# Optimization experiments

Measured on AMD Instinct MI355X. Metric: run time of the kernel, lower is better.

The kernel has to match this reference:

```python
import jax, jax.numpy as jnp
import numpy as np

N_NODES = 100000

def setup_inputs() -> dict:
    key = jax.random.key(0)
    k1, k2 = jax.random.split(key)
    node_features = jax.random.normal(k1, (N_NODES, 64), dtype=jnp.float32)
    edge_index = jax.random.randint(k2, (2, 1600000), 0, N_NODES, dtype=jnp.int64)
    return {"node_features": node_features, "edge_index": edge_index}


def reference(node_features, edge_index):
    # Gather: [E, d] source and destination node features
    src = node_features[edge_index[0]]
    dest = node_features[edge_index[1]]
    # Message: m_ij = src + dest   (minimal concrete message fn)
    messages = src + dest
    num_nodes = node_features.shape[0]
    target = edge_index[1]
    # Aggregate: scatter-add over destination node (index_add equivalent)
    aggregated = jax.ops.segment_sum(messages, target, num_segments=num_nodes)
    # aggr == 'mean': divide by in-degree, clamped at 1
    ones = jnp.ones((messages.shape[0],), dtype=messages.dtype)
    counts = jax.ops.segment_sum(ones, target, num_segments=num_nodes)
    aggregated = aggregated / jnp.clip(counts, 1.0)[:, None]
    # Update: residual (shapes match, no batchnorm/dropout)
    return node_features + aggregated
```

## Files before the change

### kernel.cpp

```cpp
#include <hip/hip_runtime.h>


#define D 64
#define NPB 32
#define NPB_SHIFT 5
#define SRC_BITS 17
#define CAP 768
#define K_BLOCKS 256
#define K_THREADS 512
#define CHUNK 1024


__global__ void detect_idx_width(const int* __restrict__ ei, int* __restrict__ flag) {
    unsigned long long nz = __ballot(ei[2 * (int)threadIdx.x + 1] != 0);
    if (threadIdx.x == 0) *flag = (nz == 0ULL) ? 1 : 0;
}

__device__ __forceinline__ int load_src(const int* ei, int e, int n_edges, bool is64) {
    return is64 ? ei[2 * (size_t)e] : ei[e];
}
__device__ __forceinline__ int load_tgt(const int* ei, int e, int n_edges, bool is64) {
    return is64 ? ei[2 * ((size_t)n_edges + e)] : ei[(size_t)n_edges + e];
}


__global__ __launch_bounds__(K_THREADS) void place_padded(
        const int* __restrict__ ei, const int* __restrict__ flag,
        int* __restrict__ gcnt, int* __restrict__ bucket, int n_edges, int nb) {
    extern __shared__ int sh[];
    int* lhist = sh;
    int* lbase = sh + nb;
    int* lcur  = sh + 2 * nb;
    const bool is64 = (*flag != 0);
    const int epb = (n_edges + gridDim.x - 1) / gridDim.x;
    const int e0 = blockIdx.x * epb;
    const int e1 = min(n_edges, e0 + epb);

    for (int i = threadIdx.x; i < nb; i += blockDim.x) { lhist[i] = 0; lcur[i] = 0; }
    __syncthreads();
    for (int e = e0 + threadIdx.x; e < e1; e += blockDim.x)
        atomicAdd(&lhist[load_tgt(ei, e, n_edges, is64) >> NPB_SHIFT], 1);
    __syncthreads();
    for (int b = threadIdx.x; b < nb; b += blockDim.x) {
        int c = lhist[b];
        lbase[b] = c ? (b * CAP + atomicAdd(&gcnt[b], c)) : 0;
    }
    __syncthreads();
    for (int e = e0 + threadIdx.x; e < e1; e += blockDim.x) {
        int s = load_src(ei, e, n_edges, is64);
        int t = load_tgt(ei, e, n_edges, is64);
        int b = t >> NPB_SHIFT;
        int pos = lbase[b] + atomicAdd(&lcur[b], 1);
        if (pos < (b + 1) * CAP)
            bucket[pos] = ((t & (NPB - 1)) << SRC_BITS) | s;
    }
}


__global__ __launch_bounds__(256) void bucket_aggregate(
        const float* __restrict__ nf, const int* __restrict__ gcnt,
        const int* __restrict__ bucket, float* __restrict__ out, int n_nodes) {
    __shared__ int st[CHUNK];
    __shared__ int srt[CHUNK];
    __shared__ int bins[NPB], ofs[NPB], cur[NPB];
    const int blk = blockIdx.x;
    const int base = blk * NPB;
    const int tid = threadIdx.x;
    const int wid = tid >> 6;
    const int lane = tid & 63;
    const int SMASK = (1 << SRC_BITS) - 1;

    float acc[8];
    int cnt[8];
#pragma unroll
    for (int k = 0; k < 8; ++k) { acc[k] = 0.f; cnt[k] = 0; }

    const int s0 = blk * CAP;
    const int m = min(gcnt[blk], CAP);

    for (int done = 0; done < m; done += CHUNK) {
        const int mc = min(CHUNK, m - done);
        if (tid < NPB) bins[tid] = 0;
        __syncthreads();
        for (int i = tid; i < mc; i += 256) {
            int p = bucket[s0 + done + i];
            st[i] = p;
            atomicAdd(&bins[p >> SRC_BITS], 1);
        }
        __syncthreads();
        if (tid < NPB) {
            int v = bins[tid];
            int incl = v;
#pragma unroll
            for (int off = 1; off < NPB; off <<= 1) {
                int up = __shfl_up(incl, off, NPB);
                if (tid >= off) incl += up;
            }
            ofs[tid] = incl - v;
            cur[tid] = incl - v;
        }
        __syncthreads();
        for (int i = tid; i < mc; i += 256) {
            int p = st[i];
            int b = p >> SRC_BITS;
            int pos = atomicAdd(&cur[b], 1);
            srt[pos] = p & SMASK;
        }
        __syncthreads();
#pragma unroll
        for (int k = 0; k < 8; ++k) {
            int r = (wid << 3) + k;
            int j0 = ofs[r];
            int n = bins[r];
            int j1 = j0 + n;
            cnt[k] += n;
            int j = j0;
            for (; j + 8 <= j1; j += 8) {
                int a0 = srt[j],     a1 = srt[j + 1], a2 = srt[j + 2], a3 = srt[j + 3];
                int a4 = srt[j + 4], a5 = srt[j + 5], a6 = srt[j + 6], a7 = srt[j + 7];
                float v0 = nf[(size_t)a0 * D + lane];
                float v1 = nf[(size_t)a1 * D + lane];
                float v2 = nf[(size_t)a2 * D + lane];
                float v3 = nf[(size_t)a3 * D + lane];
                float v4 = nf[(size_t)a4 * D + lane];
                float v5 = nf[(size_t)a5 * D + lane];
                float v6 = nf[(size_t)a6 * D + lane];
                float v7 = nf[(size_t)a7 * D + lane];
                acc[k] += v0; acc[k] += v1; acc[k] += v2; acc[k] += v3;
                acc[k] += v4; acc[k] += v5; acc[k] += v6; acc[k] += v7;
            }
            for (; j + 4 <= j1; j += 4) {
                int a0 = srt[j], a1 = srt[j + 1], a2 = srt[j + 2], a3 = srt[j + 3];
                float v0 = nf[(size_t)a0 * D + lane];
                float v1 = nf[(size_t)a1 * D + lane];
                float v2 = nf[(size_t)a2 * D + lane];
                float v3 = nf[(size_t)a3 * D + lane];
                acc[k] += v0; acc[k] += v1; acc[k] += v2; acc[k] += v3;
            }
            for (; j < j1; ++j) acc[k] += nf[(size_t)srt[j] * D + lane];
        }
        __syncthreads();
    }

#pragma unroll
    for (int k = 0; k < 8; ++k) {
        int node = base + (wid << 3) + k;
        if (node < n_nodes) {
            float c = (float)cnt[k];
            float self = nf[(size_t)node * D + lane];
            float scale = (c > 0.f) ? 2.0f : 1.0f;
            float inv = (c > 0.f) ? (1.0f / c) : 1.0f;
            out[(size_t)node * D + lane] = self * scale + acc[k] * inv;
        }
    }
}


__global__ __launch_bounds__(256) void edge_scatter(
        const float* __restrict__ nf, const int* __restrict__ ei,
        const int* __restrict__ flag, float* __restrict__ agg,
        int* __restrict__ cnt, int n_edges) {
    const bool is64 = (*flag != 0);
    const int lane = threadIdx.x & 63;
    const int wave = (int)((blockIdx.x * (unsigned)blockDim.x + threadIdx.x) >> 6);
    const int nwaves = (int)((gridDim.x * (unsigned)blockDim.x) >> 6);
    for (int e = wave; e < n_edges; e += nwaves) {
        int s = load_src(ei, e, n_edges, is64);
        int t = load_tgt(ei, e, n_edges, is64);
        atomicAdd(&agg[(size_t)t * D + lane], nf[(size_t)s * D + lane]);
        if (lane == 0) atomicAdd(&cnt[t], 1);
    }
}

__global__ __launch_bounds__(256) void finalize(
        const float* __restrict__ nf, const int* __restrict__ cnt,
        float* __restrict__ out, int n_elems) {
    int i = blockIdx.x * blockDim.x + threadIdx.x;
    if (i >= n_elems) return;
    int v = i >> 6;
    float c = (float)cnt[v];
    float inv = (c > 0.f) ? (1.0f / c) : 1.0f;
    float scale = (c > 0.f) ? 2.0f : 1.0f;
    out[i] = nf[i] * scale + out[i] * inv;
}


extern "C" void kernel_launch(void* const* d_in, const int* in_sizes, int n_in,
                              void* d_out, int out_size, void* d_ws, size_t ws_size,
                              hipStream_t stream) {
    const float* nf = (const float*)d_in[0];
    const int* ei = (const int*)d_in[1];
    float* out = (float*)d_out;

    const int n_nodes = in_sizes[0] / D;
    const int n_edges = in_sizes[1] / 2;

    const int nb = (n_nodes + NPB - 1) / NPB;

    int* gcnt   = (int*)d_ws;
    int* flag   = gcnt + nb;
    int* bucket = flag + 1;
    const size_t need = ((size_t)nb * CAP + nb + 1) * sizeof(int);
    const size_t place_lds = (size_t)3 * nb * sizeof(int);

    if (ws_size >= need && n_nodes <= (1 << SRC_BITS) && place_lds <= 64 * 1024) {
        hipMemsetAsync(gcnt, 0, (size_t)nb * sizeof(int), stream);
        detect_idx_width<<<1, 64, 0, stream>>>(ei, flag);
        place_padded<<<K_BLOCKS, K_THREADS, place_lds, stream>>>(
            ei, flag, gcnt, bucket, n_edges, nb);
        bucket_aggregate<<<nb, 256, 0, stream>>>(nf, gcnt, bucket, out, n_nodes);
    } else {
        hipMemsetAsync(d_out, 0, (size_t)out_size * sizeof(float), stream);
        hipMemsetAsync(d_ws, 0, ((size_t)n_nodes + 1) * sizeof(int), stream);
        int* fcnt = (int*)d_ws;
        int* fflag = fcnt + n_nodes;
        detect_idx_width<<<1, 64, 0, stream>>>(ei, fflag);
        edge_scatter<<<2048, 256, 0, stream>>>(nf, ei, fflag, out, fcnt, n_edges);
        finalize<<<(n_nodes * D + 255) / 256, 256, 0, stream>>>(nf, fcnt, out, n_nodes * D);
    }
}
```

Baseline: 170.0 us.

## Use two-level coarse bucketing with per-block fine filtering and XCD-aware block mapping

Edges are placed into 196 coarse buckets of 512 target nodes instead of ~3125 fine buckets of 32, so the placement kernel keeps tiny static LDS histograms and issues fewer global atomics. The index-width detection moves into the placement kernel, removing one launch. Each aggregate block then scans the whole coarse bucket (about 8K entries) and ballot-compacts only the entries for its 32 nodes, which multiplies bucket reads by 16 in exchange for cheaper placement. Block IDs are remapped so consecutive fine blocks land on the same XCD, aiming for L2 reuse of the shared coarse bucket.

```diff
diff --git a/kernel.cpp b/kernel.cpp
--- a/kernel.cpp
+++ b/kernel.cpp
@@ -2,13 +2,15 @@
 
 
 #define D 64
-#define NPB 32
-#define NPB_SHIFT 5
+#define CSHIFT 9
+#define CNODES 512
+#define FSHIFT 5
+#define FNODES 32
 #define SRC_BITS 17
-#define CAP 768
+#define CAPC 9216
+#define CAPF 768
 #define K_BLOCKS 256
 #define K_THREADS 512
-#define CHUNK 1024
 
 
 __global__ void detect_idx_width(const int* __restrict__ ei, int* __restrict__ flag) {
@@ -24,132 +26,154 @@
 }
 
 
-__global__ __launch_bounds__(K_THREADS) void place_padded(
-        const int* __restrict__ ei, const int* __restrict__ flag,
-        int* __restrict__ gcnt, int* __restrict__ bucket, int n_edges, int nb) {
-    extern __shared__ int sh[];
-    int* lhist = sh;
-    int* lbase = sh + nb;
-    int* lcur  = sh + 2 * nb;
-    const bool is64 = (*flag != 0);
+__global__ __launch_bounds__(K_THREADS) void place_coarse(
+        const int* __restrict__ ei, int* __restrict__ gcnt,
+        int* __restrict__ bucket, int n_edges, int ncoarse) {
+    __shared__ int lhist[256], lbase[256], lcur[256];
+    __shared__ int is64_sh;
+    const int tid = threadIdx.x;
+    if (tid < 64) {
+        unsigned long long nz = __ballot(ei[2 * tid + 1] != 0);
+        if (tid == 0) is64_sh = (nz == 0ULL) ? 1 : 0;
+    }
+    for (int i = tid; i < ncoarse; i += blockDim.x) { lhist[i] = 0; lcur[i] = 0; }
+    __syncthreads();
+    const bool is64 = (is64_sh != 0);
     const int epb = (n_edges + gridDim.x - 1) / gridDim.x;
     const int e0 = blockIdx.x * epb;
     const int e1 = min(n_edges, e0 + epb);
 
-    for (int i = threadIdx.x; i < nb; i += blockDim.x) { lhist[i] = 0; lcur[i] = 0; }
-    __syncthreads();
-    for (int e = e0 + threadIdx.x; e < e1; e += blockDim.x)
-        atomicAdd(&lhist[load_tgt(ei, e, n_edges, is64) >> NPB_SHIFT], 1);
-    __syncthreads();
-    for (int b = threadIdx.x; b < nb; b += blockDim.x) {
+    for (int e = e0 + tid; e < e1; e += blockDim.x)
+        atomicAdd(&lhist[load_tgt(ei, e, n_edges, is64) >> CSHIFT], 1);
+    __syncthreads();
+    for (int b = tid; b < ncoarse; b += blockDim.x) {
         int c = lhist[b];
-        lbase[b] = c ? (b * CAP + atomicAdd(&gcnt[b], c)) : 0;
-    }
-    __syncthreads();
-    for (int e = e0 + threadIdx.x; e < e1; e += blockDim.x) {
+        lbase[b] = c ? (b * CAPC + atomicAdd(&gcnt[b], c)) : 0;
+    }
+    __syncthreads();
+    for (int e = e0 + tid; e < e1; e += blockDim.x) {
         int s = load_src(ei, e, n_edges, is64);
         int t = load_tgt(ei, e, n_edges, is64);
-        int b = t >> NPB_SHIFT;
+        int b = t >> CSHIFT;
         int pos = lbase[b] + atomicAdd(&lcur[b], 1);
-        if (pos < (b + 1) * CAP)
-            bucket[pos] = ((t & (NPB - 1)) << SRC_BITS) | s;
+        if (pos < (b + 1) * CAPC)
+            bucket[pos] = ((t & (CNODES - 1)) << SRC_BITS) | s;
     }
 }
 
 
 __global__ __launch_bounds__(256) void bucket_aggregate(
         const float* __restrict__ nf, const int* __restrict__ gcnt,
-        const int* __restrict__ bucket, float* __restrict__ out, int n_nodes) {
-    __shared__ int st[CHUNK];
-    __shared__ int srt[CHUNK];
-    __shared__ int bins[NPB], ofs[NPB], cur[NPB];
-    const int blk = blockIdx.x;
-    const int base = blk * NPB;
+        const int* __restrict__ bucket, float* __restrict__ out,
+        int n_nodes, int nfine) {
+    __shared__ int stq[CAPF];
+    __shared__ int srt[CAPF];
+    __shared__ int bins[FNODES], ofs[FNODES], cur[FNODES];
+    __shared__ int mcnt_sh;
     const int tid = threadIdx.x;
     const int wid = tid >> 6;
     const int lane = tid & 63;
     const int SMASK = (1 << SRC_BITS) - 1;
 
+    const int bid = blockIdx.x;
+    const int q = nfine >> 3, r8 = nfine & 7;
+    const int xcd = bid & 7, rank = bid >> 3;
+    const int w = (xcd < r8 ? xcd * (q + 1) : r8 * (q + 1) + (xcd - r8) * q) + rank;
+
+    const int c = w >> 4;
+    const int sub = w & 15;
+    const int base = w * FNODES;
+
     float acc[8];
     int cnt[8];
 #pragma unroll
     for (int k = 0; k < 8; ++k) { acc[k] = 0.f; cnt[k] = 0; }
 
-    const int s0 = blk * CAP;
-    const int m = min(gcnt[blk], CAP);
-
-    for (int done = 0; done < m; done += CHUNK) {
-        const int mc = min(CHUNK, m - done);
-        if (tid < NPB) bins[tid] = 0;
-        __syncthreads();
-        for (int i = tid; i < mc; i += 256) {
-            int p = bucket[s0 + done + i];
-            st[i] = p;
-            atomicAdd(&bins[p >> SRC_BITS], 1);
-        }
-        __syncthreads();
-        if (tid < NPB) {
-            int v = bins[tid];
-            int incl = v;
-#pragma unroll
-            for (int off = 1; off < NPB; off <<= 1) {
-                int up = __shfl_up(incl, off, NPB);
-                if (tid >= off) incl += up;
-            }
-            ofs[tid] = incl - v;
-            cur[tid] = incl - v;
-        }
-        __syncthreads();
-        for (int i = tid; i < mc; i += 256) {
-            int p = st[i];
-            int b = p >> SRC_BITS;
-            int pos = atomicAdd(&cur[b], 1);
-            srt[pos] = p & SMASK;
-        }
-        __syncthreads();
-#pragma unroll
-        for (int k = 0; k < 8; ++k) {
-            int r = (wid << 3) + k;
-            int j0 = ofs[r];
-            int n = bins[r];
-            int j1 = j0 + n;
-            cnt[k] += n;
-            int j = j0;
-            for (; j + 8 <= j1; j += 8) {
-                int a0 = srt[j],     a1 = srt[j + 1], a2 = srt[j + 2], a3 = srt[j + 3];
-                int a4 = srt[j + 4], a5 = srt[j + 5], a6 = srt[j + 6], a7 = srt[j + 7];
-                float v0 = nf[(size_t)a0 * D + lane];
-                float v1 = nf[(size_t)a1 * D + lane];
-                float v2 = nf[(size_t)a2 * D + lane];
-                float v3 = nf[(size_t)a3 * D + lane];
-                float v4 = nf[(size_t)a4 * D + lane];
-                float v5 = nf[(size_t)a5 * D + lane];
-                float v6 = nf[(size_t)a6 * D + lane];
-                float v7 = nf[(size_t)a7 * D + lane];
-                acc[k] += v0; acc[k] += v1; acc[k] += v2; acc[k] += v3;
-                acc[k] += v4; acc[k] += v5; acc[k] += v6; acc[k] += v7;
-            }
-            for (; j + 4 <= j1; j += 4) {
-                int a0 = srt[j], a1 = srt[j + 1], a2 = srt[j + 2], a3 = srt[j + 3];
-                float v0 = nf[(size_t)a0 * D + lane];
-                float v1 = nf[(size_t)a1 * D + lane];
-                float v2 = nf[(size_t)a2 * D + lane];
-                float v3 = nf[(size_t)a3 * D + lane];
-                acc[k] += v0; acc[k] += v1; acc[k] += v2; acc[k] += v3;
-            }
-            for (; j < j1; ++j) acc[k] += nf[(size_t)srt[j] * D + lane];
-        }
-        __syncthreads();
+    if (tid == 0) mcnt_sh = 0;
+    if (tid < FNODES) bins[tid] = 0;
+    __syncthreads();
+
+    const int m = min(gcnt[c], CAPC);
+    const size_t c0 = (size_t)c * CAPC;
+    for (int i = tid; i < m; i += 256) {
+        int p = bucket[c0 + i];
+        int tl = p >> SRC_BITS;
+        bool match = ((tl >> FSHIFT) == sub);
+        unsigned long long mk = __ballot(match);
+        int wbase = 0;
+        if (lane == 0) wbase = atomicAdd(&mcnt_sh, (int)__popcll(mk));
+        wbase = __shfl(wbase, 0, 64);
+        if (match) {
+            int pos = wbase + (int)__popcll(mk & ((1ULL << lane) - 1ULL));
+            if (pos < CAPF)
+                stq[pos] = ((tl & (FNODES - 1)) << SRC_BITS) | (p & SMASK);
+        }
+    }
+    __syncthreads();
+    const int mm = min(mcnt_sh, CAPF);
+
+    for (int i = tid; i < mm; i += 256) atomicAdd(&bins[stq[i] >> SRC_BITS], 1);
+    __syncthreads();
+    if (tid < FNODES) {
+        int v = bins[tid];
+        int incl = v;
+#pragma unroll
+        for (int off = 1; off < FNODES; off <<= 1) {
+            int up = __shfl_up(incl, off, FNODES);
+            if (tid >= off) incl += up;
+        }
+        ofs[tid] = incl - v;
+        cur[tid] = incl - v;
+    }
+    __syncthreads();
+    for (int i = tid; i < mm; i += 256) {
+        int p = stq[i];
+        int pos = atomicAdd(&cur[p >> SRC_BITS], 1);
+        srt[pos] = p & SMASK;
+    }
+    __syncthreads();
+
+#pragma unroll
+    for (int k = 0; k < 8; ++k) {
+        int r = (wid << 3) + k;
+        int j0 = ofs[r];
+        int n = bins[r];
+        int j1 = j0 + n;
+        cnt[k] += n;
+        int j = j0;
+        for (; j + 8 <= j1; j += 8) {
+            int a0 = srt[j],     a1 = srt[j + 1], a2 = srt[j + 2], a3 = srt[j + 3];
+            int a4 = srt[j + 4], a5 = srt[j + 5], a6 = srt[j + 6], a7 = srt[j + 7];
+            float v0 = nf[(size_t)a0 * D + lane];
+            float v1 = nf[(size_t)a1 * D + lane];
+            float v2 = nf[(size_t)a2 * D + lane];
+            float v3 = nf[(size_t)a3 * D + lane];
+            float v4 = nf[(size_t)a4 * D + lane];
+            float v5 = nf[(size_t)a5 * D + lane];
+            float v6 = nf[(size_t)a6 * D + lane];
+            float v7 = nf[(size_t)a7 * D + lane];
+            acc[k] += v0; acc[k] += v1; acc[k] += v2; acc[k] += v3;
+            acc[k] += v4; acc[k] += v5; acc[k] += v6; acc[k] += v7;
+        }
+        for (; j + 4 <= j1; j += 4) {
+            int a0 = srt[j], a1 = srt[j + 1], a2 = srt[j + 2], a3 = srt[j + 3];
+            float v0 = nf[(size_t)a0 * D + lane];
+            float v1 = nf[(size_t)a1 * D + lane];
+            float v2 = nf[(size_t)a2 * D + lane];
+            float v3 = nf[(size_t)a3 * D + lane];
+            acc[k] += v0; acc[k] += v1; acc[k] += v2; acc[k] += v3;
+        }
+        for (; j < j1; ++j) acc[k] += nf[(size_t)srt[j] * D + lane];
     }
 
 #pragma unroll
     for (int k = 0; k < 8; ++k) {
         int node = base + (wid << 3) + k;
         if (node < n_nodes) {
-            float c = (float)cnt[k];
+            float cc = (float)cnt[k];
             float self = nf[(size_t)node * D + lane];
-            float scale = (c > 0.f) ? 2.0f : 1.0f;
-            float inv = (c > 0.f) ? (1.0f / c) : 1.0f;
+            float scale = (cc > 0.f) ? 2.0f : 1.0f;
+            float inv = (cc > 0.f) ? (1.0f / cc) : 1.0f;
             out[(size_t)node * D + lane] = self * scale + acc[k] * inv;
         }
     }
@@ -195,20 +219,20 @@
     const int n_nodes = in_sizes[0] / D;
     const int n_edges = in_sizes[1] / 2;
 
-    const int nb = (n_nodes + NPB - 1) / NPB;
+    const int ncoarse = (n_nodes + CNODES - 1) / CNODES;
+    const int nfine   = (n_nodes + FNODES - 1) / FNODES;
 
     int* gcnt   = (int*)d_ws;
-    int* flag   = gcnt + nb;
+    int* flag   = gcnt + ncoarse;
     int* bucket = flag + 1;
-    const size_t need = ((size_t)nb * CAP + nb + 1) * sizeof(int);
-    const size_t place_lds = (size_t)3 * nb * sizeof(int);
-
-    if (ws_size >= need && n_nodes <= (1 << SRC_BITS) && place_lds <= 64 * 1024) {
-        hipMemsetAsync(gcnt, 0, (size_t)nb * sizeof(int), stream);
-        detect_idx_width<<<1, 64, 0, stream>>>(ei, flag);
-        place_padded<<<K_BLOCKS, K_THREADS, place_lds, stream>>>(
-            ei, flag, gcnt, bucket, n_edges, nb);
-        bucket_aggregate<<<nb, 256, 0, stream>>>(nf, gcnt, bucket, out, n_nodes);
+    const size_t need = ((size_t)ncoarse * CAPC + ncoarse + 1) * sizeof(int);
+
+    if (ws_size >= need && n_nodes <= (1 << SRC_BITS) && ncoarse <= 256) {
+        hipMemsetAsync(gcnt, 0, (size_t)ncoarse * sizeof(int), stream);
+        place_coarse<<<K_BLOCKS, K_THREADS, 0, stream>>>(
+            ei, gcnt, bucket, n_edges, ncoarse);
+        bucket_aggregate<<<nfine, 256, 0, stream>>>(
+            nf, gcnt, bucket, out, n_nodes, nfine);
     } else {
         hipMemsetAsync(d_out, 0, (size_t)out_size * sizeof(float), stream);
         hipMemsetAsync(d_ws, 0, ((size_t)n_nodes + 1) * sizeof(int), stream);
```

New measurement: 180.5 us. +6.1%, slower.

## Stash edges in registers during placement and fuse index-width detection

Applied to the files above, without the earlier changes.

The placement kernel now assigns a fixed 4096 edges to each 1024-thread block. Each thread loads its four edges once, keeps the packed values in registers, and builds the histogram in the same pass, so the second read of edge_index is gone. The separate index-width detection launch is folded into each placement block, which removes one kernel launch. LDS use drops to two arrays because the histogram array is reused as the cursor. In exchange there are many more blocks (about 391), each doing its own global gcnt atomics over all buckets, which adds contention and repeated bucket scans.

```diff
diff --git a/kernel.cpp b/kernel.cpp
--- a/kernel.cpp
+++ b/kernel.cpp
@@ -6,9 +6,9 @@
 #define NPB_SHIFT 5
 #define SRC_BITS 17
 #define CAP 768
-#define K_BLOCKS 256
-#define K_THREADS 512
 #define CHUNK 1024
+#define EPB 4096
+#define P_THREADS 1024
 
 
 __global__ void detect_idx_width(const int* __restrict__ ei, int* __restrict__ flag) {
@@ -24,35 +24,83 @@
 }
 
 
-__global__ __launch_bounds__(K_THREADS) void place_padded(
-        const int* __restrict__ ei, const int* __restrict__ flag,
-        int* __restrict__ gcnt, int* __restrict__ bucket, int n_edges, int nb) {
+__global__ __launch_bounds__(P_THREADS) void place_stash(
+        const int* __restrict__ ei, int* __restrict__ gcnt,
+        int* __restrict__ bucket, int n_edges, int nb) {
     extern __shared__ int sh[];
-    int* lhist = sh;
+    int* lh    = sh;
     int* lbase = sh + nb;
-    int* lcur  = sh + 2 * nb;
-    const bool is64 = (*flag != 0);
-    const int epb = (n_edges + gridDim.x - 1) / gridDim.x;
-    const int e0 = blockIdx.x * epb;
-    const int e1 = min(n_edges, e0 + epb);
-
-    for (int i = threadIdx.x; i < nb; i += blockDim.x) { lhist[i] = 0; lcur[i] = 0; }
+    __shared__ int is64_sh;
+    const int tid = threadIdx.x;
+
+    if (tid < 64) {
+        unsigned long long nz = __ballot(ei[2 * tid + 1] != 0);
+        if (tid == 0) is64_sh = (nz == 0ULL) ? 1 : 0;
+    }
+    for (int i = tid; i < nb; i += P_THREADS) lh[i] = 0;
     __syncthreads();
-    for (int e = e0 + threadIdx.x; e < e1; e += blockDim.x)
-        atomicAdd(&lhist[load_tgt(ei, e, n_edges, is64) >> NPB_SHIFT], 1);
+    const bool is64 = (is64_sh != 0);
+    const int e0 = blockIdx.x * EPB;
+    const int e1 = min(n_edges, e0 + EPB);
+
+    int pk0 = 0, pk1 = 0, pk2 = 0, pk3 = 0;
+    int bk0 = -1, bk1 = -1, bk2 = -1, bk3 = -1;
+    {
+        int e = e0 + tid;
+        if (e < e1) {
+            int s = load_src(ei, e, n_edges, is64);
+            int t = load_tgt(ei, e, n_edges, is64);
+            bk0 = t >> NPB_SHIFT;
+            pk0 = ((t & (NPB - 1)) << SRC_BITS) | s;
+            atomicAdd(&lh[bk0], 1);
+        }
+        e += P_THREADS;
+        if (e < e1) {
+            int s = load_src(ei, e, n_edges, is64);
+            int t = load_tgt(ei, e, n_edges, is64);
+            bk1 = t >> NPB_SHIFT;
+            pk1 = ((t & (NPB - 1)) << SRC_BITS) | s;
+            atomicAdd(&lh[bk1], 1);
+        }
+        e += P_THREADS;
+        if (e < e1) {
+            int s = load_src(ei, e, n_edges, is64);
+            int t = load_tgt(ei, e, n_edges, is64);
+            bk2 = t >> NPB_SHIFT;
+            pk2 = ((t & (NPB - 1)) << SRC_BITS) | s;
+            atomicAdd(&lh[bk2], 1);
+        }
+        e += P_THREADS;
+        if (e < e1) {
+            int s = load_src(ei, e, n_edges, is64);
+            int t = load_tgt(ei, e, n_edges, is64);
+            bk3 = t >> NPB_SHIFT;
+            pk3 = ((t & (NPB - 1)) << SRC_BITS) | s;
+            atomicAdd(&lh[bk3], 1);
+        }
+    }
     __syncthreads();
-    for (int b = threadIdx.x; b < nb; b += blockDim.x) {
-        int c = lhist[b];
+    for (int b = tid; b < nb; b += P_THREADS) {
+        int c = lh[b];
         lbase[b] = c ? (b * CAP + atomicAdd(&gcnt[b], c)) : 0;
+        lh[b] = 0;
     }
     __syncthreads();
-    for (int e = e0 + threadIdx.x; e < e1; e += blockDim.x) {
-        int s = load_src(ei, e, n_edges, is64);
-        int t = load_tgt(ei, e, n_edges, is64);
-        int b = t >> NPB_SHIFT;
-        int pos = lbase[b] + atomicAdd(&lcur[b], 1);
-        if (pos < (b + 1) * CAP)
-            bucket[pos] = ((t & (NPB - 1)) << SRC_BITS) | s;
+    if (bk0 >= 0) {
+        int pos = lbase[bk0] + atomicAdd(&lh[bk0], 1);
+        if (pos < (bk0 + 1) * CAP) bucket[pos] = pk0;
+    }
+    if (bk1 >= 0) {
+        int pos = lbase[bk1] + atomicAdd(&lh[bk1], 1);
+        if (pos < (bk1 + 1) * CAP) bucket[pos] = pk1;
+    }
+    if (bk2 >= 0) {
+        int pos = lbase[bk2] + atomicAdd(&lh[bk2], 1);
+        if (pos < (bk2 + 1) * CAP) bucket[pos] = pk2;
+    }
+    if (bk3 >= 0) {
+        int pos = lbase[bk3] + atomicAdd(&lh[bk3], 1);
+        if (pos < (bk3 + 1) * CAP) bucket[pos] = pk3;
     }
 }
 
@@ -102,8 +150,7 @@
         __syncthreads();
         for (int i = tid; i < mc; i += 256) {
             int p = st[i];
-            int b = p >> SRC_BITS;
-            int pos = atomicAdd(&cur[b], 1);
+            int pos = atomicAdd(&cur[p >> SRC_BITS], 1);
             srt[pos] = p & SMASK;
         }
         __syncthreads();
@@ -201,13 +248,13 @@
     int* flag   = gcnt + nb;
     int* bucket = flag + 1;
     const size_t need = ((size_t)nb * CAP + nb + 1) * sizeof(int);
-    const size_t place_lds = (size_t)3 * nb * sizeof(int);
+    const size_t place_lds = (size_t)2 * nb * sizeof(int);
 
     if (ws_size >= need && n_nodes <= (1 << SRC_BITS) && place_lds <= 64 * 1024) {
         hipMemsetAsync(gcnt, 0, (size_t)nb * sizeof(int), stream);
-        detect_idx_width<<<1, 64, 0, stream>>>(ei, flag);
-        place_padded<<<K_BLOCKS, K_THREADS, place_lds, stream>>>(
-            ei, flag, gcnt, bucket, n_edges, nb);
+        const int nblk = (n_edges + EPB - 1) / EPB;
+        place_stash<<<nblk, P_THREADS, place_lds, stream>>>(
+            ei, gcnt, bucket, n_edges, nb);
         bucket_aggregate<<<nb, 256, 0, stream>>>(nf, gcnt, bucket, out, n_nodes);
     } else {
         hipMemsetAsync(d_out, 0, (size_t)out_size * sizeof(float), stream);
```

After: 166.4 us. 2.1% less time.
